# Performance work log

Measured on AMD Instinct MI355X. Metric: run time of the kernel, lower is better.

The kernel has to match this reference:

```python
import jax, jax.numpy as jnp
import numpy as np
from jax import lax

E = 1024      # embed_dim
H = 16        # num_heads
HD = E // H   # head_dim = 64
GS = 2        # head_group_size
G = H // GS   # num head groups = 8
KQ = 3        # kq kernel q size
KK = 3        # kq kernel k size


def setup_inputs() -> dict:
    key = jax.random.key(0)
    ks = jax.random.split(key, 18)
    B, S = 2, 1024
    def rn(k, shape, scale=1.0):
        return jax.random.normal(k, shape, dtype=jnp.float32) * scale
    return {
        "Q": rn(ks[0], (B, S, E)),
        "K": rn(ks[1], (B, S, E)),
        "V": rn(ks[2], (B, S, E)),
        "Wq": rn(ks[3], (E, E), 0.02), "bq": rn(ks[4], (E,), 0.02),
        "Wk": rn(ks[5], (E, E), 0.02), "bk": rn(ks[6], (E,), 0.02),
        "Wv": rn(ks[7], (E, E), 0.02), "bv": rn(ks[8], (E,), 0.02),
        "Wo": rn(ks[9], (E, E), 0.02), "bo": rn(ks[10], (E,), 0.02),
        # depthwise key-query conv: [out=H, in/groups=1, KQ, KK]
        "kq_w": rn(ks[11], (H, 1, KQ, KK), 0.1),
        "kq_b": rn(ks[12], (H,), 0.02),
        # grouped 1x1 head-mix conv: weight [H, GS] (kernel dim squeezed), bias [H]
        "mix_w": rn(ks[13], (H, GS), 0.3),
        "mix_b": rn(ks[14], (H,), 0.02),
        # DynamicTanh params over head_dim (channels_last)
        "dyt_alpha": jnp.array([0.5], dtype=jnp.float32),
        "dyt_w": jnp.ones((HD,), dtype=jnp.float32),
        "dyt_b": jnp.zeros((HD,), dtype=jnp.float32),
        "depth_scale": jnp.ones((1,), dtype=jnp.float32),
    }


def reference(Q, K, V, Wq, bq, Wk, bk, Wv, bv, Wo, bo,
              kq_w, kq_b, mix_w, mix_b, dyt_alpha, dyt_w, dyt_b, depth_scale):
    B, S, _ = Q.shape
    scale = HD ** (-0.5)
    # projections -> [B, H, S, HD]
    q = (Q @ Wq + bq).reshape(B, S, H, HD).transpose(0, 2, 1, 3)
    k = (K @ Wk + bk).reshape(B, S, H, HD).transpose(0, 2, 1, 3)
    v = (V @ Wv + bv).reshape(B, S, H, HD).transpose(0, 2, 1, 3)

    # raw logits [B, H, Sq, Sk], multiplicative causal mask (zeros above diag)
    logits = jnp.einsum('bhqd,bhkd->bhqk', q, k) * scale
    causal = jnp.tril(jnp.ones((S, S), dtype=logits.dtype))
    logits = logits * causal

    # per-head (depthwise) key-query conv2d; torch pads q-dim by 2 both sides
    # then crops to first S rows (causal in q), k-dim padded symmetrically by 1
    conv = lax.conv_general_dilated(
        logits, kq_w, window_strides=(1, 1),
        padding=[(KQ - 1, KQ - 1), ((KK - 1) // 2, (KK - 1) // 2)],
        dimension_numbers=('NCHW', 'OIHW', 'NCHW'),
        feature_group_count=H)
    conv = conv + kq_b[None, :, None, None]
    conv = conv[:, :, :S, :]

    attn = jax.nn.softmax(conv, axis=-1)

    # grouped 1x1 head-mixing conv (within groups of GS heads) + bias
    attn_g = attn.reshape(B, G, GS, S, S)
    mw = mix_w.reshape(G, GS, GS)  # [group, out_in_group, in_in_group]
    mixed = jnp.einsum('goj,bgjqk->bgoqk', mw, attn_g).reshape(B, H, S, S)
    mixed = mixed + mix_b[None, :, None, None]

    out = jnp.einsum('bhqk,bhkd->bhqd', mixed, v)
    # DynamicTanh over head_dim (channels_last) + depth scale
    out = jnp.tanh(dyt_alpha * out) * dyt_w + dyt_b
    out = out * depth_scale
    out = out.transpose(0, 2, 1, 3).reshape(B, S, E)
    return out @ Wo + bo
```

## Files before the change

### kernel.cpp

```cpp
#include <hip/hip_runtime.h>
#include <cstdint>
#include <cstddef>

typedef __bf16 bf16;
typedef __bf16 bf16x8 __attribute__((ext_vector_type(8)));
typedef float f32x4 __attribute__((ext_vector_type(4)));

#define DEVI static __device__ __forceinline__

DEVI unsigned int cvt_pk_bf16(float lo, float hi) {
  unsigned int bl = __float_as_uint(lo);
  bl += 0x7fffu + ((bl >> 16) & 1u);
  unsigned int bh = __float_as_uint(hi);
  bh += 0x7fffu + ((bh >> 16) & 1u);
  return (bl >> 16) | (bh & 0xffff0000u);
}
DEVI float bf_lo(unsigned int u) { return __uint_as_float(u << 16); }
DEVI float bf_hi(unsigned int u) { return __uint_as_float(u & 0xffff0000u); }

DEVI void gload16(const bf16* g, bf16* l) {
  __builtin_amdgcn_global_load_lds(
      (const __attribute__((address_space(1))) unsigned int*)g,
      (__attribute__((address_space(3))) unsigned int*)l, 16, 0, 0);
}

__global__ __launch_bounds__(256) void prep_k(
    const float* __restrict__ Wq, const float* __restrict__ Wk,
    const float* __restrict__ Wv, const float* __restrict__ Wo,
    const float* __restrict__ Q, const float* __restrict__ K,
    const float* __restrict__ V, bf16* __restrict__ Wt,
    bf16* __restrict__ Ab)
{
  __shared__ bf16 Ts[64 * 72];
  const int bid = blockIdx.x, tid = threadIdx.x;
  if (bid < 1024) {
    const int z = bid >> 8;
    const float* W = (z == 0) ? Wq : (z == 1) ? Wk : (z == 2) ? Wv : Wo;
    bf16* out = Wt + ((size_t)z << 20);
    const int n0 = (bid & 15) * 64, k0 = ((bid >> 4) & 15) * 64;
    #pragma unroll
    for (int i = 0; i < 4; ++i) {
      int t = tid + i * 256;
      int kr = t >> 4, nc = t & 15;
      float4 v = *(const float4*)(W + (size_t)(k0 + kr) * 1024 + n0 + nc * 4);
      Ts[(nc * 4 + 0) * 72 + kr] = (bf16)v.x;
      Ts[(nc * 4 + 1) * 72 + kr] = (bf16)v.y;
      Ts[(nc * 4 + 2) * 72 + kr] = (bf16)v.z;
      Ts[(nc * 4 + 3) * 72 + kr] = (bf16)v.w;
    }
    __syncthreads();
    const int n = tid >> 2, kc = tid & 3;
    *(uint4*)(out + (size_t)(n0 + n) * 1024 + k0 + kc * 16) =
        *(const uint4*)(&Ts[n * 72 + kc * 16]);
    *(uint4*)(out + (size_t)(n0 + n) * 1024 + k0 + kc * 16 + 8) =
        *(const uint4*)(&Ts[n * 72 + kc * 16 + 8]);
  } else {
    const int t = bid - 1024;
    const int z = t >> 10, x = t & 1023;
    const float* A = (z == 0) ? Q : (z == 1) ? K : V;
    bf16* o = Ab + ((size_t)z << 21);
    const size_t idx = (size_t)x * 256 + tid;
    const float4 v0 = *(const float4*)(A + idx * 8);
    const float4 v1 = *(const float4*)(A + idx * 8 + 4);
    uint4 u;
    u.x = cvt_pk_bf16(v0.x, v0.y);
    u.y = cvt_pk_bf16(v0.z, v0.w);
    u.z = cvt_pk_bf16(v1.x, v1.y);
    u.w = cvt_pk_bf16(v1.z, v1.w);
    *(uint4*)(o + idx * 8) = u;
  }
}

__global__ __launch_bounds__(256) void proj_gemm_k(
    const bf16* __restrict__ Ab, const bf16* __restrict__ Wt,
    const float* __restrict__ bq, const float* __restrict__ bk,
    const float* __restrict__ bv, bf16* __restrict__ outbase,
    float* __restrict__ Tsum)
{
  const int z = blockIdx.z;
  const bf16* A  = Ab + ((size_t)z << 21);
  const bf16* Bt = Wt + ((size_t)z << 20);
  const float* bias = (z == 0) ? bq : (z == 1) ? bk : bv;
  bf16* outb = outbase + ((size_t)z << 21);

  __shared__ __align__(16) bf16 Asm[2][8192];
  __shared__ __align__(16) bf16 Bsm[2][4096];

  const int tid = threadIdx.x, lane = tid & 63, wid = tid >> 6;
  const int q4 = lane >> 4, n16 = lane & 15;
  const int wm = wid >> 1, wn = wid & 1;
  const int bid = blockIdx.x;
  const int m0 = (bid & 15) * 128, n0 = (bid >> 4) * 64;

  const int cbase = wid * 64 + lane;
  const bf16* gA[4];
  #pragma unroll
  for (int i = 0; i < 4; ++i) {
    int cc = cbase + i * 256;
    gA[i] = A + (size_t)(m0 + (cc >> 3)) * 1024 + (((cc & 7) ^ ((cc >> 3) & 7)) << 3);
  }
  const bf16* gB[2];
  #pragma unroll
  for (int i = 0; i < 2; ++i) {
    int cc = cbase + i * 256;
    gB[i] = Bt + (size_t)(n0 + (cc >> 3)) * 1024 + (((cc & 7) ^ ((cc >> 3) & 7)) << 3);
  }
  const int swl = n16 & 7;

  f32x4 acc[4][2] = {};

  #pragma unroll
  for (int i = 0; i < 4; ++i) gload16(gA[i], &Asm[0][i * 2048 + wid * 512]);
  #pragma unroll
  for (int i = 0; i < 2; ++i) gload16(gB[i], &Bsm[0][i * 2048 + wid * 512]);
  __syncthreads();

  int cur = 0;
  for (int t = 0; t < 16; ++t) {
    if (t < 15) {
      const int kc = (t + 1) * 64;
      #pragma unroll
      for (int i = 0; i < 4; ++i) gload16(gA[i] + kc, &Asm[cur ^ 1][i * 2048 + wid * 512]);
      #pragma unroll
      for (int i = 0; i < 2; ++i) gload16(gB[i] + kc, &Bsm[cur ^ 1][i * 2048 + wid * 512]);
    }
    const char* ab = (const char*)&Asm[cur][0];
    const char* bb = (const char*)&Bsm[cur][0];
    bf16x8 af[2][4], bfv[2][2];
    #pragma unroll
    for (int kk2 = 0; kk2 < 2; ++kk2) {
      #pragma unroll
      for (int rt = 0; rt < 4; ++rt)
        af[kk2][rt] = *(const bf16x8*)(ab + (wm * 64 + rt * 16 + n16) * 128 +
                                       (((kk2 * 4 + q4) ^ swl) << 4));
      #pragma unroll
      for (int ct = 0; ct < 2; ++ct)
        bfv[kk2][ct] = *(const bf16x8*)(bb + (wn * 32 + ct * 16 + n16) * 128 +
                                        (((kk2 * 4 + q4) ^ swl) << 4));
    }
    #pragma unroll
    for (int kk2 = 0; kk2 < 2; ++kk2)
      #pragma unroll
      for (int rt = 0; rt < 4; ++rt)
        #pragma unroll
        for (int ct = 0; ct < 2; ++ct)
          acc[rt][ct] = __builtin_amdgcn_mfma_f32_16x16x32_bf16(af[kk2][rt], bfv[kk2][ct], acc[rt][ct], 0, 0, 0);
    __syncthreads();
    cur ^= 1;
  }

  if (z < 2) {
    const int h = n0 >> 6;
    #pragma unroll
    for (int ct = 0; ct < 2; ++ct) {
      const int dl = wn * 32 + ct * 16 + n16;
      const float bvl = bias[n0 + dl];
      #pragma unroll
      for (int rt = 0; rt < 4; ++rt) {
        #pragma unroll
        for (int r = 0; r < 4; ++r) {
          int row = m0 + wm * 64 + rt * 16 + q4 * 4 + r;
          int b2 = row >> 10, s = row & 1023;
          outb[((size_t)((b2 * 16 + h) * 1024 + s) << 6) + dl] =
              (bf16)(acc[rt][ct][r] + bvl);
        }
      }
    }
  } else {
    const int b2 = m0 >> 10, kt0 = (m0 & 1023) >> 6, hh = n0 >> 6;
    bf16* vout = outb + ((size_t)(b2 * 16 + hh) << 16) + (size_t)(kt0 + wm) * 4096;
    float csum[2] = {0.f, 0.f};
    #pragma unroll
    for (int rt = 0; rt < 4; ++rt) {
      const int kk = rt >> 1;
      const int q4c = (rt & 1) * 2 + (q4 >> 1);
      const int jo = (q4 & 1) * 4;
      #pragma unroll
      for (int ct = 0; ct < 2; ++ct) {
        const int cl = wn * 32 + ct * 16 + n16;
        const float bvl = bias[n0 + cl];
        unsigned int p0 = cvt_pk_bf16(acc[rt][ct][0] + bvl, acc[rt][ct][1] + bvl);
        unsigned int p1 = cvt_pk_bf16(acc[rt][ct][2] + bvl, acc[rt][ct][3] + bvl);
        csum[ct] += bf_lo(p0) + bf_hi(p0) + bf_lo(p1) + bf_hi(p1);
        *(uint2*)(vout + kk * 2048 + (wn * 2 + ct) * 512 + (q4c * 16 + n16) * 8 + jo) =
            make_uint2(p0, p1);
      }
    }
    #pragma unroll
    for (int ct = 0; ct < 2; ++ct) {
      csum[ct] += __shfl_xor(csum[ct], 16);
      csum[ct] += __shfl_xor(csum[ct], 32);
    }
    if (lane < 16) {
      float* tsd = Tsum + ((size_t)(b2 * 16 + hh) * 16 + kt0 + wm) * 64 + wn * 32 + n16;
      tsd[0]  = csum[0];
      tsd[16] = csum[1];
    }
  }
}

__global__ __launch_bounds__(256) void out_gemm_k(
    const bf16* __restrict__ Ab, const bf16* __restrict__ Bt,
    const float* __restrict__ bias, float* __restrict__ outf)
{
  __shared__ __align__(16) bf16 Asm[2][4096];
  __shared__ __align__(16) bf16 Bsm[2][4096];
  const int tid = threadIdx.x, lane = tid & 63, wid = tid >> 6;
  const int q4 = lane >> 4, n16 = lane & 15;
  const int wm = wid >> 1, wn = wid & 1;
  const int bid = blockIdx.x;
  const int m0 = (bid & 31) * 64, n0 = (bid >> 5) * 64;
  const int cbase = wid * 64 + lane;
  const bf16* gA[2];
  const bf16* gB[2];
  #pragma unroll
  for (int i = 0; i < 2; ++i) {
    int cc = cbase + i * 256;
    gA[i] = Ab + (size_t)(m0 + (cc >> 3)) * 1024 + (((cc & 7) ^ ((cc >> 3) & 7)) << 3);
    gB[i] = Bt + (size_t)(n0 + (cc >> 3)) * 1024 + (((cc & 7) ^ ((cc >> 3) & 7)) << 3);
  }
  const int swl = n16 & 7;
  f32x4 acc[2][2] = {};

  #pragma unroll
  for (int i = 0; i < 2; ++i) {
    gload16(gA[i], &Asm[0][i * 2048 + wid * 512]);
    gload16(gB[i], &Bsm[0][i * 2048 + wid * 512]);
  }
  __syncthreads();

  int cur = 0;
  for (int t = 0; t < 16; ++t) {
    if (t < 15) {
      const int kc = (t + 1) * 64;
      #pragma unroll
      for (int i = 0; i < 2; ++i) {
        gload16(gA[i] + kc, &Asm[cur ^ 1][i * 2048 + wid * 512]);
        gload16(gB[i] + kc, &Bsm[cur ^ 1][i * 2048 + wid * 512]);
      }
    }
    const char* ab = (const char*)&Asm[cur][0];
    const char* bb = (const char*)&Bsm[cur][0];
    bf16x8 af[2][2], bfv[2][2];
    #pragma unroll
    for (int kk2 = 0; kk2 < 2; ++kk2) {
      #pragma unroll
      for (int rt = 0; rt < 2; ++rt)
        af[kk2][rt] = *(const bf16x8*)(ab + (wm * 32 + rt * 16 + n16) * 128 +
                                       (((kk2 * 4 + q4) ^ swl) << 4));
      #pragma unroll
      for (int ct = 0; ct < 2; ++ct)
        bfv[kk2][ct] = *(const bf16x8*)(bb + (wn * 32 + ct * 16 + n16) * 128 +
                                        (((kk2 * 4 + q4) ^ swl) << 4));
    }
    #pragma unroll
    for (int kk2 = 0; kk2 < 2; ++kk2)
      #pragma unroll
      for (int rt = 0; rt < 2; ++rt)
        #pragma unroll
        for (int ct = 0; ct < 2; ++ct)
          acc[rt][ct] = __builtin_amdgcn_mfma_f32_16x16x32_bf16(af[kk2][rt], bfv[kk2][ct], acc[rt][ct], 0, 0, 0);
    __syncthreads();
    cur ^= 1;
  }
  #pragma unroll
  for (int ct = 0; ct < 2; ++ct) {
    int col = n0 + wn * 32 + ct * 16 + n16;
    float bvl = bias[col];
    #pragma unroll
    for (int rt = 0; rt < 2; ++rt)
      #pragma unroll
      for (int r = 0; r < 4; ++r) {
        int row = m0 + wm * 32 + rt * 16 + q4 * 4 + r;
        outf[(size_t)row * 1024 + col] = acc[rt][ct][r] + bvl;
      }
  }
}

__global__ __launch_bounds__(320) void logits_conv_k(
    const bf16* __restrict__ qh, const bf16* __restrict__ kh,
    const float* __restrict__ kq_w, const float* __restrict__ kq_b,
    bf16* __restrict__ conv_out, float* __restrict__ tstats,
    const float* __restrict__ Tsum, float* __restrict__ Vtail)
{
  const int tt = blockIdx.x;
  const int h = blockIdx.y, b = blockIdx.z;
  if (tt == 151) {
    const int d = threadIdx.x;
    if (d < 64) {
      float* vt = Vtail + (size_t)(b * 16 + h) * 17 * 64;
      vt[16 * 64 + d] = 0.f;
      float c = 0.f;
      for (int kt = 15; kt >= 0; --kt) {
        c += Tsum[((size_t)(b * 16 + h) * 16 + kt) * 64 + d];
        vt[kt * 64 + d] = c;
      }
    }
    return;
  }
  int qt = 0, base = 0;
  while (qt < 15 && base + qt + 2 <= tt) { base += qt + 2; ++qt; }
  const int ct = tt - base;
  const int q0 = qt * 64, c0 = ct * 64;
  __shared__ __align__(16) char un[19456];
  bf16* Kst = (bf16*)un;
  float* Ls = (float*)un;
  const int tid = threadIdx.x;
  const int lane = tid & 63, wid = tid >> 6;
  const int q4 = lane >> 4, n16 = lane & 15;
  const bf16* qb = qh + ((size_t)(b * 16 + h) << 16);
  const bf16* kb = kh + ((size_t)(b * 16 + h) << 16);

  const int ar = min(max(q0 - 2 + wid * 16 + n16, 0), 1023);
  bf16x8 a0 = *(const bf16x8*)(qb + ar * 64 + q4 * 8);
  bf16x8 a1 = *(const bf16x8*)(qb + ar * 64 + 32 + q4 * 8);

  for (int t = tid; t < 640; t += 320) {
    int row = t >> 3, ch = t & 7;
    int br = min(max(c0 - 1 + row, 0), 1023);
    *(uint4*)(&Kst[row * 72 + ch * 8]) = *(const uint4*)(kb + br * 64 + ch * 8);
  }
  __syncthreads();

  f32x4 acc[5] = {};
  #pragma unroll
  for (int c5 = 0; c5 < 5; ++c5) {
    int brow = c5 * 16 + n16;
    bf16x8 b0 = *(const bf16x8*)(&Kst[brow * 72 + q4 * 8]);
    bf16x8 b1 = *(const bf16x8*)(&Kst[brow * 72 + 32 + q4 * 8]);
    acc[c5] = __builtin_amdgcn_mfma_f32_16x16x32_bf16(a0, b0, acc[c5], 0, 0, 0);
    acc[c5] = __builtin_amdgcn_mfma_f32_16x16x32_bf16(a1, b1, acc[c5], 0, 0, 0);
  }
  __syncthreads();

  #pragma unroll
  for (int c5 = 0; c5 < 5; ++c5) {
    #pragma unroll
    for (int r = 0; r < 4; ++r) {
      int Lrow = wid * 16 + q4 * 4 + r;
      int Lcol = c5 * 16 + n16;
      if (Lrow < 66 && Lcol < 66) {
        int rg = q0 - 2 + Lrow;
        int cg = c0 - 1 + Lcol;
        float v = (cg >= 0 && cg <= rg) ? acc[c5][r] * 0.125f : 0.f;
        Ls[Lrow * 72 + Lcol] = v;
      }
    }
  }
  __syncthreads();

  if (tid < 256) {
    float w9[9];
    #pragma unroll
    for (int i = 0; i < 9; ++i) w9[i] = kq_w[h * 9 + i];
    const float bb = kq_b[h];
    const size_t tplane = (size_t)(b * 16 + h) * 151 + base + ct;
    bf16* tb = conv_out + tplane * 4096;
    float2* st = (float2*)tstats + tplane * 64;

    const int r = tid >> 2, qr = tid & 3;
    float4 R0[5], R1[5], R2[5];
    const float* L0 = &Ls[r * 72 + qr * 16];
    #pragma unroll
    for (int i = 0; i < 5; ++i) {
      R0[i] = *(const float4*)(L0 + i * 4);
      R1[i] = *(const float4*)(L0 + 72 + i * 4);
      R2[i] = *(const float4*)(L0 + 144 + i * 4);
    }
    const float* f0 = (const float*)R0;
    const float* f1 = (const float*)R1;
    const float* f2 = (const float*)R2;
    float o[16];
    #pragma unroll
    for (int jj = 0; jj < 16; ++jj)
      o[jj] = bb + w9[0]*f0[jj] + w9[1]*f0[jj+1] + w9[2]*f0[jj+2]
                 + w9[3]*f1[jj] + w9[4]*f1[jj+1] + w9[5]*f1[jj+2]
                 + w9[6]*f2[jj] + w9[7]*f2[jj+1] + w9[8]*f2[jj+2];
    float mx = o[0];
    #pragma unroll
    for (int jj = 1; jj < 16; ++jj) mx = fmaxf(mx, o[jj]);
    mx = fmaxf(mx, __shfl_xor(mx, 1));
    mx = fmaxf(mx, __shfl_xor(mx, 2));
    unsigned int p[8];
    #pragma unroll
    for (int jj = 0; jj < 8; ++jj)
      p[jj] = cvt_pk_bf16(__expf(o[2*jj] - mx), __expf(o[2*jj+1] - mx));
    const int kk = qr >> 1, q4b = (qr & 1) * 2, sr = r >> 4, n16r = r & 15;
    *(uint4*)(tb + (sr * 2 + kk) * 512 + (q4b * 16 + n16r) * 8)       = *(const uint4*)&p[0];
    *(uint4*)(tb + (sr * 2 + kk) * 512 + ((q4b + 1) * 16 + n16r) * 8) = *(const uint4*)&p[4];
    float s = 0.f;
    #pragma unroll
    for (int jj = 0; jj < 8; ++jj) s += bf_lo(p[jj]) + bf_hi(p[jj]);
    s += __shfl_xor(s, 1);
    s += __shfl_xor(s, 2);
    if (qr == 0) st[r] = make_float2(mx, s);
  }
}

__global__ __launch_bounds__(256) void pv_k(
    const bf16* __restrict__ conv_out, const bf16* __restrict__ V2,
    const float* __restrict__ tstats, const float* __restrict__ Vtail,
    const float* __restrict__ mix_w, const float* __restrict__ mix_b,
    const float* __restrict__ kq_b,
    const float* __restrict__ dyt_alpha, const float* __restrict__ dyt_w,
    const float* __restrict__ dyt_b, const float* __restrict__ depth_scale,
    bf16* __restrict__ out_attn)
{
  const int qt16 = blockIdx.x, g = blockIdx.y, b = blockIdx.z;
  const int qt = qt16 >> 2;
  const int nkt = min(qt + 2, 16);
  const int Tc = 1024 - (nkt << 6);
  const int tid = threadIdx.x, lane = tid & 63, wid = tid >> 6;
  const int q4 = lane >> 4, n16 = lane & 15;
  const int h0 = 2 * g;
  const int sr = qt16 & 3, strow = sr * 16;
  const size_t tbase = (size_t)(qt * (qt + 3) / 2);

  __shared__ float2 rsS[2][16];
  if (tid < 32) {
    const int hh = tid >> 4, rw = tid & 15;
    const float2* tsp = (const float2*)tstats +
        ((size_t)(b * 16 + h0 + hh) * 151 + tbase) * 64 + strow + rw;
    const float kb2 = kq_b[h0 + hh];
    float mx = (Tc > 0) ? kb2 : -3.0e38f;
    for (int kt = 0; kt < nkt; ++kt) mx = fmaxf(mx, tsp[(size_t)kt * 64].x);
    float s = (float)Tc * __expf(kb2 - mx);
    for (int kt = 0; kt < nkt; ++kt) {
      float2 v = tsp[(size_t)kt * 64];
      s += v.y * __expf(v.x - mx);
    }
    rsS[hh][rw] = make_float2(mx, 1.f / s);
  }
  __syncthreads();

  const float m0v = rsS[0][n16].x, m1v = rsS[1][n16].x;
  const float ri0 = rsS[0][n16].y, ri1 = rsS[1][n16].y;
  const float c00 = mix_w[(h0 + 0) * 2 + 0] * ri0, c01 = mix_w[(h0 + 0) * 2 + 1] * ri1;
  const float c10 = mix_w[(h0 + 1) * 2 + 0] * ri0, c11 = mix_w[(h0 + 1) * 2 + 1] * ri1;

  const bf16* pb0 = conv_out +
      ((size_t)(b * 16 + h0) * 151 + tbase) * 4096 + sr * 1024 + lane * 8;
  const bf16* pb1 = pb0 + (size_t)151 * 4096;
  const float2* ts0 = (const float2*)tstats +
      ((size_t)(b * 16 + h0) * 151 + tbase) * 64 + strow + n16;
  const float2* ts1 = ts0 + (size_t)151 * 64;
  const bf16* vb0 = V2 + ((size_t)(b * 16 + h0) << 16) + lane * 8;
  const bf16* vb1 = vb0 + ((size_t)1 << 16);

  f32x4 acc0[4] = {}, acc1[4] = {};
  for (int kt = wid; kt < nkt; kt += 4) {
    uint4 u0[2], u1[2];
    #pragma unroll
    for (int kk = 0; kk < 2; ++kk) {
      u0[kk] = *(const uint4*)(pb0 + (size_t)kt * 4096 + kk * 512);
      u1[kk] = *(const uint4*)(pb1 + (size_t)kt * 4096 + kk * 512);
    }
    const float e0 = __expf(ts0[(size_t)kt * 64].x - m0v);
    const float e1 = __expf(ts1[(size_t)kt * 64].x - m1v);
    const float w00 = c00 * e0, w01 = c01 * e1;
    const float w10 = c10 * e0, w11 = c11 * e1;
    #pragma unroll
    for (int kk = 0; kk < 2; ++kk) {
      bf16x8 bv0[4], bv1[4];
      #pragma unroll
      for (int ctt = 0; ctt < 4; ++ctt) {
        bv0[ctt] = *(const bf16x8*)(vb0 + (size_t)kt * 4096 + kk * 2048 + ctt * 512);
        bv1[ctt] = *(const bf16x8*)(vb1 + (size_t)kt * 4096 + kk * 2048 + ctt * 512);
      }
      bf16x8 af0, af1;
      const unsigned int* a0p = (const unsigned int*)&u0[kk];
      const unsigned int* a1p = (const unsigned int*)&u1[kk];
      #pragma unroll
      for (int i2 = 0; i2 < 4; ++i2) {
        const float plo = bf_lo(a0p[i2]), phi = bf_hi(a0p[i2]);
        const float qlo = bf_lo(a1p[i2]), qhi = bf_hi(a1p[i2]);
        ((unsigned int*)&af0)[i2] = cvt_pk_bf16(w00 * plo + w01 * qlo,
                                                w00 * phi + w01 * qhi);
        ((unsigned int*)&af1)[i2] = cvt_pk_bf16(w10 * plo + w11 * qlo,
                                                w10 * phi + w11 * qhi);
      }
      #pragma unroll
      for (int ctt = 0; ctt < 4; ++ctt) {
        acc0[ctt] = __builtin_amdgcn_mfma_f32_16x16x32_bf16(af0, bv0[ctt], acc0[ctt], 0, 0, 0);
        acc1[ctt] = __builtin_amdgcn_mfma_f32_16x16x32_bf16(af1, bv1[ctt], acc1[ctt], 0, 0, 0);
      }
    }
  }

  __shared__ float Ps[8][16][65];
  #pragma unroll
  for (int ctt = 0; ctt < 4; ++ctt)
    #pragma unroll
    for (int r = 0; r < 4; ++r) {
      Ps[wid * 2 + 0][q4 * 4 + r][ctt * 16 + n16] = acc0[ctt][r];
      Ps[wid * 2 + 1][q4 * 4 + r][ctt * 16 + n16] = acc1[ctt][r];
    }
  __syncthreads();

  const int o = tid >> 7, rem = tid & 127, row = rem >> 3, cg = rem & 7;
  const float2 sA = rsS[0][row], sB = rsS[1][row];
  const float kqb0 = kq_b[h0], kqb1 = kq_b[h0 + 1];
  const float mwa = mix_w[(h0 + o) * 2 + 0], mwb = mix_w[(h0 + o) * 2 + 1];
  const float twr = (Tc > 0) ? (mwa * sA.y * __expf(kqb0 - sA.x) +
                                mwb * sB.y * __expf(kqb1 - sB.x)) : 0.f;
  const float mb = mix_b[h0 + o];
  const float alpha = dyt_alpha[0], dsc = depth_scale[0];
  const float* vt = Vtail + (size_t)(b * 16 + h0 + o) * 17 * 64;
  bf16 outv[8];
  #pragma unroll
  for (int j = 0; j < 8; ++j) {
    const int d = cg * 8 + j;
    float s = Ps[0 * 2 + o][row][d] + Ps[1 * 2 + o][row][d] +
              Ps[2 * 2 + o][row][d] + Ps[3 * 2 + o][row][d];
    float v = s + twr * vt[(size_t)nkt * 64 + d] + mb * vt[d];
    float e = __expf(2.f * alpha * v);
    float th = 1.f - 2.f / (e + 1.f);
    float y = (th * dyt_w[d] + dyt_b[d]) * dsc;
    outv[j] = (bf16)y;
  }
  const int qr = qt16 * 16 + row;
  *(uint4*)(out_attn + (((size_t)(b * 1024 + qr)) << 10) + (h0 + o) * 64 + cg * 8) =
      *(const uint4*)outv;
}

extern "C" void kernel_launch(void* const* d_in, const int* in_sizes, int n_in,
                              void* d_out, int out_size, void* d_ws, size_t ws_size,
                              hipStream_t stream) {
  const float* Q    = (const float*)d_in[0];
  const float* Kx   = (const float*)d_in[1];
  const float* V    = (const float*)d_in[2];
  const float* Wq   = (const float*)d_in[3];
  const float* bq   = (const float*)d_in[4];
  const float* Wk   = (const float*)d_in[5];
  const float* bk   = (const float*)d_in[6];
  const float* Wv   = (const float*)d_in[7];
  const float* bv   = (const float*)d_in[8];
  const float* Wo   = (const float*)d_in[9];
  const float* bo   = (const float*)d_in[10];
  const float* kq_w = (const float*)d_in[11];
  const float* kq_b = (const float*)d_in[12];
  const float* mixw = (const float*)d_in[13];
  const float* mixb = (const float*)d_in[14];
  const float* dyta = (const float*)d_in[15];
  const float* dytw = (const float*)d_in[16];
  const float* dytb = (const float*)d_in[17];
  const float* dsc  = (const float*)d_in[18];

  char* ws = (char*)d_ws;
  bf16* qh     = (bf16*)(ws);
  float* tstat = (float*)(ws + (size_t)(12 << 20));
  float* Vtail = (float*)(ws + (size_t)(16 << 20));
  float* Tsum  = (float*)(ws + (size_t)(16 << 20) + (256 << 10));
  bf16* WtT    = (bf16*)(ws + (size_t)(17 << 20));
  bf16* oat    = (bf16*)(ws + (size_t)(17 << 20));
  bf16* conv   = (bf16*)(ws + (size_t)(25 << 20));
  bf16* Ab     = (bf16*)(ws + (size_t)(25 << 20));
  bf16* kh     = qh + ((size_t)1 << 21);
  bf16* V2     = qh + ((size_t)2 << 21);

  prep_k<<<dim3(4096), 256, 0, stream>>>(Wq, Wk, Wv, Wo, Q, Kx, V, WtT, Ab);
  proj_gemm_k<<<dim3(256, 1, 3), 256, 0, stream>>>(Ab, WtT, bq, bk, bv, qh, Tsum);
  logits_conv_k<<<dim3(152, 16, 2), 320, 0, stream>>>(qh, kh, kq_w, kq_b, conv, tstat,
                                                      Tsum, Vtail);
  pv_k<<<dim3(64, 8, 2), 256, 0, stream>>>(conv, V2, tstat, Vtail, mixw, mixb, kq_b,
                                           dyta, dytw, dytb, dsc, oat);
  out_gemm_k<<<dim3(512), 256, 0, stream>>>(oat, WtT + ((size_t)3 << 20), bo, (float*)d_out);
}
```

Before: 209.6 us.

## Fuse logits, conv, softmax and PV into a flash-style online-softmax kernel

Replaces the two-pass design, which wrote bf16 conv tiles and per-tile stats to global memory and reread them in a separate PV kernel, with one kernel per (query tile, head). That kernel loops over key tiles, keeps the softmax normalised online, and multiplies P by V for both its own head and its pair head. A small mix kernel then applies the grouped head mixing, the DynamicTanh and the tail corrections. This removes the large intermediate traffic. In exchange the grid shrinks to 512 blocks with an uneven causal workload, each key-tile step has serial barriers, P·V work doubles, and fp32 Xs/Xc buffers are written out.

```diff
diff --git a/kernel.cpp b/kernel.cpp
--- a/kernel.cpp
+++ b/kernel.cpp
@@ -277,250 +277,235 @@
   }
 }
 
-__global__ __launch_bounds__(320) void logits_conv_k(
+__global__ __launch_bounds__(320) void fattn_k(
     const bf16* __restrict__ qh, const bf16* __restrict__ kh,
-    const float* __restrict__ kq_w, const float* __restrict__ kq_b,
-    bf16* __restrict__ conv_out, float* __restrict__ tstats,
-    const float* __restrict__ Tsum, float* __restrict__ Vtail)
+    const bf16* __restrict__ V2, const float* __restrict__ kq_w,
+    const float* __restrict__ kq_b, const float* __restrict__ Tsum,
+    float* __restrict__ Xs, float* __restrict__ Xc)
 {
-  const int tt = blockIdx.x;
   const int h = blockIdx.y, b = blockIdx.z;
-  if (tt == 151) {
-    const int d = threadIdx.x;
-    if (d < 64) {
-      float* vt = Vtail + (size_t)(b * 16 + h) * 17 * 64;
-      vt[16 * 64 + d] = 0.f;
-      float c = 0.f;
-      for (int kt = 15; kt >= 0; --kt) {
-        c += Tsum[((size_t)(b * 16 + h) * 16 + kt) * 64 + d];
-        vt[kt * 64 + d] = c;
-      }
-    }
-    return;
-  }
-  int qt = 0, base = 0;
-  while (qt < 15 && base + qt + 2 <= tt) { base += qt + 2; ++qt; }
-  const int ct = tt - base;
-  const int q0 = qt * 64, c0 = ct * 64;
+  const int ph = h ^ 1;
+  const int qt = b ? (15 - blockIdx.x) : blockIdx.x;
+  const int q0 = qt * 64;
+  const int nkt = min(qt + 2, 16);
+  const int Tc = 1024 - (nkt << 6);
   __shared__ __align__(16) char un[19456];
   bf16* Kst = (bf16*)un;
   float* Ls = (float*)un;
-  const int tid = threadIdx.x;
-  const int lane = tid & 63, wid = tid >> 6;
+  __shared__ __align__(16) bf16 Pls[4096];
+  __shared__ float mLds[64], lLds[64], fLds[64], vtnLds[64], vtn2Lds[64];
+
+  const int tid = threadIdx.x, lane = tid & 63, wid = tid >> 6;
   const int q4 = lane >> 4, n16 = lane & 15;
   const bf16* qb = qh + ((size_t)(b * 16 + h) << 16);
-  const bf16* kb = kh + ((size_t)(b * 16 + h) << 16);
+  const bf16* kp = kh + ((size_t)(b * 16 + h) << 16);
+  const bf16* vb  = V2 + ((size_t)(b * 16 + h)  << 16) + lane * 8;
+  const bf16* vb2 = V2 + ((size_t)(b * 16 + ph) << 16) + lane * 8;
+  const float kqb = kq_b[h];
 
   const int ar = min(max(q0 - 2 + wid * 16 + n16, 0), 1023);
   bf16x8 a0 = *(const bf16x8*)(qb + ar * 64 + q4 * 8);
   bf16x8 a1 = *(const bf16x8*)(qb + ar * 64 + 32 + q4 * 8);
 
-  for (int t = tid; t < 640; t += 320) {
-    int row = t >> 3, ch = t & 7;
-    int br = min(max(c0 - 1 + row, 0), 1023);
-    *(uint4*)(&Kst[row * 72 + ch * 8]) = *(const uint4*)(kb + br * 64 + ch * 8);
-  }
+  float w9[9];
+  #pragma unroll
+  for (int i = 0; i < 9; ++i) w9[i] = kq_w[h * 9 + i];
+
+  if (tid < 64) {
+    mLds[tid] = -3.0e38f;
+    lLds[tid] = 0.f;
+    float s = 0.f, s2 = 0.f;
+    for (int k2 = nkt; k2 < 16; ++k2) {
+      s  += Tsum[((size_t)(b * 16 + h)  * 16 + k2) * 64 + tid];
+      s2 += Tsum[((size_t)(b * 16 + ph) * 16 + k2) * 64 + tid];
+    }
+    vtnLds[tid] = s;
+    vtn2Lds[tid] = s2;
+  }
+  f32x4 accp[4] = {}, accq[4] = {};
   __syncthreads();
 
-  f32x4 acc[5] = {};
-  #pragma unroll
-  for (int c5 = 0; c5 < 5; ++c5) {
-    int brow = c5 * 16 + n16;
-    bf16x8 b0 = *(const bf16x8*)(&Kst[brow * 72 + q4 * 8]);
-    bf16x8 b1 = *(const bf16x8*)(&Kst[brow * 72 + 32 + q4 * 8]);
-    acc[c5] = __builtin_amdgcn_mfma_f32_16x16x32_bf16(a0, b0, acc[c5], 0, 0, 0);
-    acc[c5] = __builtin_amdgcn_mfma_f32_16x16x32_bf16(a1, b1, acc[c5], 0, 0, 0);
-  }
-  __syncthreads();
-
-  #pragma unroll
-  for (int c5 = 0; c5 < 5; ++c5) {
-    #pragma unroll
-    for (int r = 0; r < 4; ++r) {
-      int Lrow = wid * 16 + q4 * 4 + r;
-      int Lcol = c5 * 16 + n16;
-      if (Lrow < 66 && Lcol < 66) {
-        int rg = q0 - 2 + Lrow;
-        int cg = c0 - 1 + Lcol;
-        float v = (cg >= 0 && cg <= rg) ? acc[c5][r] * 0.125f : 0.f;
-        Ls[Lrow * 72 + Lcol] = v;
-      }
-    }
-  }
-  __syncthreads();
+  for (int kt = 0; kt < nkt; ++kt) {
+    const int c0 = kt * 64;
+    for (int t = tid; t < 640; t += 320) {
+      int row = t >> 3, ch = t & 7;
+      int br = min(max(c0 - 1 + row, 0), 1023);
+      *(uint4*)(&Kst[row * 72 + ch * 8]) = *(const uint4*)(kp + br * 64 + ch * 8);
+    }
+    __syncthreads();
+
+    f32x4 acc[5] = {};
+    #pragma unroll
+    for (int c5 = 0; c5 < 5; ++c5) {
+      int brow = c5 * 16 + n16;
+      bf16x8 b0 = *(const bf16x8*)(&Kst[brow * 72 + q4 * 8]);
+      bf16x8 b1 = *(const bf16x8*)(&Kst[brow * 72 + 32 + q4 * 8]);
+      acc[c5] = __builtin_amdgcn_mfma_f32_16x16x32_bf16(a0, b0, acc[c5], 0, 0, 0);
+      acc[c5] = __builtin_amdgcn_mfma_f32_16x16x32_bf16(a1, b1, acc[c5], 0, 0, 0);
+    }
+    __syncthreads();
+
+    #pragma unroll
+    for (int c5 = 0; c5 < 5; ++c5) {
+      #pragma unroll
+      for (int r = 0; r < 4; ++r) {
+        int Lrow = wid * 16 + q4 * 4 + r;
+        int Lcol = c5 * 16 + n16;
+        if (Lrow < 66 && Lcol < 66) {
+          int rg = q0 - 2 + Lrow;
+          int cg = c0 - 1 + Lcol;
+          float v = (cg >= 0 && cg <= rg) ? acc[c5][r] * 0.125f : 0.f;
+          Ls[Lrow * 72 + Lcol] = v;
+        }
+      }
+    }
+    __syncthreads();
+
+    if (tid < 256) {
+      const int r = tid >> 2, qr = tid & 3;
+      float4 R0[5], R1[5], R2[5];
+      const float* L0 = &Ls[r * 72 + qr * 16];
+      #pragma unroll
+      for (int i = 0; i < 5; ++i) {
+        R0[i] = *(const float4*)(L0 + i * 4);
+        R1[i] = *(const float4*)(L0 + 72 + i * 4);
+        R2[i] = *(const float4*)(L0 + 144 + i * 4);
+      }
+      const float* f0 = (const float*)R0;
+      const float* f1 = (const float*)R1;
+      const float* f2 = (const float*)R2;
+      float o[16];
+      #pragma unroll
+      for (int jj = 0; jj < 16; ++jj)
+        o[jj] = kqb + w9[0]*f0[jj] + w9[1]*f0[jj+1] + w9[2]*f0[jj+2]
+                    + w9[3]*f1[jj] + w9[4]*f1[jj+1] + w9[5]*f1[jj+2]
+                    + w9[6]*f2[jj] + w9[7]*f2[jj+1] + w9[8]*f2[jj+2];
+      float mx = o[0];
+      #pragma unroll
+      for (int jj = 1; jj < 16; ++jj) mx = fmaxf(mx, o[jj]);
+      mx = fmaxf(mx, __shfl_xor(mx, 1));
+      mx = fmaxf(mx, __shfl_xor(mx, 2));
+      const float m_old = mLds[r];
+      const float m_new = fmaxf(m_old, mx);
+      const float fsc = __expf(m_old - m_new);
+      unsigned int p[8];
+      #pragma unroll
+      for (int jj = 0; jj < 8; ++jj)
+        p[jj] = cvt_pk_bf16(__expf(o[2*jj] - m_new), __expf(o[2*jj+1] - m_new));
+      const int kk = qr >> 1, q4b = (qr & 1) * 2, sr = r >> 4, n16r = r & 15;
+      *(uint4*)(Pls + (sr * 2 + kk) * 512 + (q4b * 16 + n16r) * 8)       = *(const uint4*)&p[0];
+      *(uint4*)(Pls + (sr * 2 + kk) * 512 + ((q4b + 1) * 16 + n16r) * 8) = *(const uint4*)&p[4];
+      float s = 0.f;
+      #pragma unroll
+      for (int jj = 0; jj < 8; ++jj) s += bf_lo(p[jj]) + bf_hi(p[jj]);
+      s += __shfl_xor(s, 1);
+      s += __shfl_xor(s, 2);
+      if (qr == 0) {
+        lLds[r] = lLds[r] * fsc + s;
+        mLds[r] = m_new;
+        fLds[r] = fsc;
+      }
+    }
+    __syncthreads();
+
+    if (tid < 256) {
+      const float fr0 = fLds[wid * 16 + q4 * 4 + 0];
+      const float fr1 = fLds[wid * 16 + q4 * 4 + 1];
+      const float fr2 = fLds[wid * 16 + q4 * 4 + 2];
+      const float fr3 = fLds[wid * 16 + q4 * 4 + 3];
+      #pragma unroll
+      for (int ctt = 0; ctt < 4; ++ctt) {
+        accp[ctt][0] *= fr0; accp[ctt][1] *= fr1;
+        accp[ctt][2] *= fr2; accp[ctt][3] *= fr3;
+        accq[ctt][0] *= fr0; accq[ctt][1] *= fr1;
+        accq[ctt][2] *= fr2; accq[ctt][3] *= fr3;
+      }
+      bf16x8 pa0 = *(const bf16x8*)(Pls + (wid * 2 + 0) * 512 + lane * 8);
+      bf16x8 pa1 = *(const bf16x8*)(Pls + (wid * 2 + 1) * 512 + lane * 8);
+      #pragma unroll
+      for (int ctt = 0; ctt < 4; ++ctt) {
+        bf16x8 bv0 = *(const bf16x8*)(vb + (size_t)kt * 4096 + ctt * 512);
+        bf16x8 bv1 = *(const bf16x8*)(vb + (size_t)kt * 4096 + 2048 + ctt * 512);
+        accp[ctt] = __builtin_amdgcn_mfma_f32_16x16x32_bf16(pa0, bv0, accp[ctt], 0, 0, 0);
+        accp[ctt] = __builtin_amdgcn_mfma_f32_16x16x32_bf16(pa1, bv1, accp[ctt], 0, 0, 0);
+        bf16x8 cv0 = *(const bf16x8*)(vb2 + (size_t)kt * 4096 + ctt * 512);
+        bf16x8 cv1 = *(const bf16x8*)(vb2 + (size_t)kt * 4096 + 2048 + ctt * 512);
+        accq[ctt] = __builtin_amdgcn_mfma_f32_16x16x32_bf16(pa0, cv0, accq[ctt], 0, 0, 0);
+        accq[ctt] = __builtin_amdgcn_mfma_f32_16x16x32_bf16(pa1, cv1, accq[ctt], 0, 0, 0);
+      }
+    }
+  }
 
   if (tid < 256) {
-    float w9[9];
-    #pragma unroll
-    for (int i = 0; i < 9; ++i) w9[i] = kq_w[h * 9 + i];
-    const float bb = kq_b[h];
-    const size_t tplane = (size_t)(b * 16 + h) * 151 + base + ct;
-    bf16* tb = conv_out + tplane * 4096;
-    float2* st = (float2*)tstats + tplane * 64;
-
-    const int r = tid >> 2, qr = tid & 3;
-    float4 R0[5], R1[5], R2[5];
-    const float* L0 = &Ls[r * 72 + qr * 16];
-    #pragma unroll
-    for (int i = 0; i < 5; ++i) {
-      R0[i] = *(const float4*)(L0 + i * 4);
-      R1[i] = *(const float4*)(L0 + 72 + i * 4);
-      R2[i] = *(const float4*)(L0 + 144 + i * 4);
-    }
-    const float* f0 = (const float*)R0;
-    const float* f1 = (const float*)R1;
-    const float* f2 = (const float*)R2;
-    float o[16];
-    #pragma unroll
-    for (int jj = 0; jj < 16; ++jj)
-      o[jj] = bb + w9[0]*f0[jj] + w9[1]*f0[jj+1] + w9[2]*f0[jj+2]
-                 + w9[3]*f1[jj] + w9[4]*f1[jj+1] + w9[5]*f1[jj+2]
-                 + w9[6]*f2[jj] + w9[7]*f2[jj+1] + w9[8]*f2[jj+2];
-    float mx = o[0];
-    #pragma unroll
-    for (int jj = 1; jj < 16; ++jj) mx = fmaxf(mx, o[jj]);
-    mx = fmaxf(mx, __shfl_xor(mx, 1));
-    mx = fmaxf(mx, __shfl_xor(mx, 2));
-    unsigned int p[8];
-    #pragma unroll
-    for (int jj = 0; jj < 8; ++jj)
-      p[jj] = cvt_pk_bf16(__expf(o[2*jj] - mx), __expf(o[2*jj+1] - mx));
-    const int kk = qr >> 1, q4b = (qr & 1) * 2, sr = r >> 4, n16r = r & 15;
-    *(uint4*)(tb + (sr * 2 + kk) * 512 + (q4b * 16 + n16r) * 8)       = *(const uint4*)&p[0];
-    *(uint4*)(tb + (sr * 2 + kk) * 512 + ((q4b + 1) * 16 + n16r) * 8) = *(const uint4*)&p[4];
-    float s = 0.f;
-    #pragma unroll
-    for (int jj = 0; jj < 8; ++jj) s += bf_lo(p[jj]) + bf_hi(p[jj]);
-    s += __shfl_xor(s, 1);
-    s += __shfl_xor(s, 2);
-    if (qr == 0) st[r] = make_float2(mx, s);
-  }
-}
-
-__global__ __launch_bounds__(256) void pv_k(
-    const bf16* __restrict__ conv_out, const bf16* __restrict__ V2,
-    const float* __restrict__ tstats, const float* __restrict__ Vtail,
+    float* As = Xs + ((size_t)(b * 16 + h) << 16);
+    float* Ac = Xc + ((size_t)(b * 16 + h) << 16);
+    #pragma unroll
+    for (int rr = 0; rr < 4; ++rr) {
+      const int row = wid * 16 + q4 * 4 + rr;
+      const float m_run = mLds[row], l_run = lLds[row];
+      float g = 1.f, eb = 0.f, l = l_run;
+      if (Tc > 0) {
+        const float mf = fmaxf(m_run, kqb);
+        g = __expf(m_run - mf);
+        eb = __expf(kqb - mf);
+        l = l_run * g + (float)Tc * eb;
+      }
+      const float rinv = 1.f / l;
+      #pragma unroll
+      for (int ctt = 0; ctt < 4; ++ctt) {
+        const int col = ctt * 16 + n16;
+        As[(size_t)(q0 + row) * 64 + col] =
+            (accp[ctt][rr] * g + eb * vtnLds[col]) * rinv;
+        Ac[(size_t)(q0 + row) * 64 + col] =
+            (accq[ctt][rr] * g + eb * vtn2Lds[col]) * rinv;
+      }
+    }
+  }
+}
+
+__global__ __launch_bounds__(256) void mix_k(
+    const float* __restrict__ Xs, const float* __restrict__ Xc,
+    const float* __restrict__ Tsum,
     const float* __restrict__ mix_w, const float* __restrict__ mix_b,
-    const float* __restrict__ kq_b,
     const float* __restrict__ dyt_alpha, const float* __restrict__ dyt_w,
     const float* __restrict__ dyt_b, const float* __restrict__ depth_scale,
-    bf16* __restrict__ out_attn)
+    bf16* __restrict__ oat)
 {
-  const int qt16 = blockIdx.x, g = blockIdx.y, b = blockIdx.z;
-  const int qt = qt16 >> 2;
-  const int nkt = min(qt + 2, 16);
-  const int Tc = 1024 - (nkt << 6);
-  const int tid = threadIdx.x, lane = tid & 63, wid = tid >> 6;
-  const int q4 = lane >> 4, n16 = lane & 15;
-  const int h0 = 2 * g;
-  const int sr = qt16 & 3, strow = sr * 16;
-  const size_t tbase = (size_t)(qt * (qt + 3) / 2);
-
-  __shared__ float2 rsS[2][16];
-  if (tid < 32) {
-    const int hh = tid >> 4, rw = tid & 15;
-    const float2* tsp = (const float2*)tstats +
-        ((size_t)(b * 16 + h0 + hh) * 151 + tbase) * 64 + strow + rw;
-    const float kb2 = kq_b[h0 + hh];
-    float mx = (Tc > 0) ? kb2 : -3.0e38f;
-    for (int kt = 0; kt < nkt; ++kt) mx = fmaxf(mx, tsp[(size_t)kt * 64].x);
-    float s = (float)Tc * __expf(kb2 - mx);
-    for (int kt = 0; kt < nkt; ++kt) {
-      float2 v = tsp[(size_t)kt * 64];
-      s += v.y * __expf(v.x - mx);
-    }
-    rsS[hh][rw] = make_float2(mx, 1.f / s);
+  const int qc = blockIdx.x, h = blockIdx.y, b = blockIdx.z;
+  const int tid = threadIdx.x;
+  __shared__ float vt0[64];
+  if (tid < 64) {
+    float s = 0.f;
+    for (int kt = 0; kt < 16; ++kt)
+      s += Tsum[((size_t)(b * 16 + h) * 16 + kt) * 64 + tid];
+    vt0[tid] = s;
   }
   __syncthreads();
-
-  const float m0v = rsS[0][n16].x, m1v = rsS[1][n16].x;
-  const float ri0 = rsS[0][n16].y, ri1 = rsS[1][n16].y;
-  const float c00 = mix_w[(h0 + 0) * 2 + 0] * ri0, c01 = mix_w[(h0 + 0) * 2 + 1] * ri1;
-  const float c10 = mix_w[(h0 + 1) * 2 + 0] * ri0, c11 = mix_w[(h0 + 1) * 2 + 1] * ri1;
-
-  const bf16* pb0 = conv_out +
-      ((size_t)(b * 16 + h0) * 151 + tbase) * 4096 + sr * 1024 + lane * 8;
-  const bf16* pb1 = pb0 + (size_t)151 * 4096;
-  const float2* ts0 = (const float2*)tstats +
-      ((size_t)(b * 16 + h0) * 151 + tbase) * 64 + strow + n16;
-  const float2* ts1 = ts0 + (size_t)151 * 64;
-  const bf16* vb0 = V2 + ((size_t)(b * 16 + h0) << 16) + lane * 8;
-  const bf16* vb1 = vb0 + ((size_t)1 << 16);
-
-  f32x4 acc0[4] = {}, acc1[4] = {};
-  for (int kt = wid; kt < nkt; kt += 4) {
-    uint4 u0[2], u1[2];
-    #pragma unroll
-    for (int kk = 0; kk < 2; ++kk) {
-      u0[kk] = *(const uint4*)(pb0 + (size_t)kt * 4096 + kk * 512);
-      u1[kk] = *(const uint4*)(pb1 + (size_t)kt * 4096 + kk * 512);
-    }
-    const float e0 = __expf(ts0[(size_t)kt * 64].x - m0v);
-    const float e1 = __expf(ts1[(size_t)kt * 64].x - m1v);
-    const float w00 = c00 * e0, w01 = c01 * e1;
-    const float w10 = c10 * e0, w11 = c11 * e1;
-    #pragma unroll
-    for (int kk = 0; kk < 2; ++kk) {
-      bf16x8 bv0[4], bv1[4];
-      #pragma unroll
-      for (int ctt = 0; ctt < 4; ++ctt) {
-        bv0[ctt] = *(const bf16x8*)(vb0 + (size_t)kt * 4096 + kk * 2048 + ctt * 512);
-        bv1[ctt] = *(const bf16x8*)(vb1 + (size_t)kt * 4096 + kk * 2048 + ctt * 512);
-      }
-      bf16x8 af0, af1;
-      const unsigned int* a0p = (const unsigned int*)&u0[kk];
-      const unsigned int* a1p = (const unsigned int*)&u1[kk];
-      #pragma unroll
-      for (int i2 = 0; i2 < 4; ++i2) {
-        const float plo = bf_lo(a0p[i2]), phi = bf_hi(a0p[i2]);
-        const float qlo = bf_lo(a1p[i2]), qhi = bf_hi(a1p[i2]);
-        ((unsigned int*)&af0)[i2] = cvt_pk_bf16(w00 * plo + w01 * qlo,
-                                                w00 * phi + w01 * qhi);
-        ((unsigned int*)&af1)[i2] = cvt_pk_bf16(w10 * plo + w11 * qlo,
-                                                w10 * phi + w11 * qhi);
-      }
-      #pragma unroll
-      for (int ctt = 0; ctt < 4; ++ctt) {
-        acc0[ctt] = __builtin_amdgcn_mfma_f32_16x16x32_bf16(af0, bv0[ctt], acc0[ctt], 0, 0, 0);
-        acc1[ctt] = __builtin_amdgcn_mfma_f32_16x16x32_bf16(af1, bv1[ctt], acc1[ctt], 0, 0, 0);
-      }
-    }
-  }
-
-  __shared__ float Ps[8][16][65];
-  #pragma unroll
-  for (int ctt = 0; ctt < 4; ++ctt)
-    #pragma unroll
-    for (int r = 0; r < 4; ++r) {
-      Ps[wid * 2 + 0][q4 * 4 + r][ctt * 16 + n16] = acc0[ctt][r];
-      Ps[wid * 2 + 1][q4 * 4 + r][ctt * 16 + n16] = acc1[ctt][r];
-    }
-  __syncthreads();
-
-  const int o = tid >> 7, rem = tid & 127, row = rem >> 3, cg = rem & 7;
-  const float2 sA = rsS[0][row], sB = rsS[1][row];
-  const float kqb0 = kq_b[h0], kqb1 = kq_b[h0 + 1];
-  const float mwa = mix_w[(h0 + o) * 2 + 0], mwb = mix_w[(h0 + o) * 2 + 1];
-  const float twr = (Tc > 0) ? (mwa * sA.y * __expf(kqb0 - sA.x) +
-                                mwb * sB.y * __expf(kqb1 - sB.x)) : 0.f;
-  const float mb = mix_b[h0 + o];
+  const int j0 = h & ~1, j1 = j0 + 1;
+  const float* A0 = ((h & 1) ? Xc : Xs) + ((size_t)(b * 16 + j0) << 16);
+  const float* A1 = ((h & 1) ? Xs : Xc) + ((size_t)(b * 16 + j1) << 16);
+  const float mw0 = mix_w[h * 2 + 0], mw1 = mix_w[h * 2 + 1], mbv = mix_b[h];
   const float alpha = dyt_alpha[0], dsc = depth_scale[0];
-  const float* vt = Vtail + (size_t)(b * 16 + h0 + o) * 17 * 64;
-  bf16 outv[8];
-  #pragma unroll
-  for (int j = 0; j < 8; ++j) {
-    const int d = cg * 8 + j;
-    float s = Ps[0 * 2 + o][row][d] + Ps[1 * 2 + o][row][d] +
-              Ps[2 * 2 + o][row][d] + Ps[3 * 2 + o][row][d];
-    float v = s + twr * vt[(size_t)nkt * 64 + d] + mb * vt[d];
-    float e = __expf(2.f * alpha * v);
-    float th = 1.f - 2.f / (e + 1.f);
-    float y = (th * dyt_w[d] + dyt_b[d]) * dsc;
-    outv[j] = (bf16)y;
-  }
-  const int qr = qt16 * 16 + row;
-  *(uint4*)(out_attn + (((size_t)(b * 1024 + qr)) << 10) + (h0 + o) * 64 + cg * 8) =
-      *(const uint4*)outv;
+  const int d0 = (tid & 15) * 4;
+  const int qoff = tid >> 4;
+  for (int rep = 0; rep < 8; ++rep) {
+    const int q = qc * 128 + rep * 16 + qoff;
+    const float4 u0 = *(const float4*)(A0 + (size_t)q * 64 + d0);
+    const float4 u1 = *(const float4*)(A1 + (size_t)q * 64 + d0);
+    const float* a0p = (const float*)&u0;
+    const float* a1p = (const float*)&u1;
+    bf16 outv[4];
+    #pragma unroll
+    for (int i = 0; i < 4; ++i) {
+      const int d = d0 + i;
+      float v = mw0 * a0p[i] + mw1 * a1p[i] + mbv * vt0[d];
+      float e = __expf(2.f * alpha * v);
+      float th = 1.f - 2.f / (e + 1.f);
+      outv[i] = (bf16)((th * dyt_w[d] + dyt_b[d]) * dsc);
+    }
+    *(uint2*)(oat + ((size_t)(b * 1024 + q) << 10) + h * 64 + d0) =
+        *(const uint2*)outv;
+  }
 }
 
 extern "C" void kernel_launch(void* const* d_in, const int* in_sizes, int n_in,
@@ -548,21 +533,19 @@
 
   char* ws = (char*)d_ws;
   bf16* qh     = (bf16*)(ws);
-  float* tstat = (float*)(ws + (size_t)(12 << 20));
-  float* Vtail = (float*)(ws + (size_t)(16 << 20));
   float* Tsum  = (float*)(ws + (size_t)(16 << 20) + (256 << 10));
   bf16* WtT    = (bf16*)(ws + (size_t)(17 << 20));
   bf16* oat    = (bf16*)(ws + (size_t)(17 << 20));
-  bf16* conv   = (bf16*)(ws + (size_t)(25 << 20));
   bf16* Ab     = (bf16*)(ws + (size_t)(25 << 20));
+  float* Xs    = (float*)(ws + (size_t)(25 << 20));
+  float* Xc    = (float*)(ws + (size_t)(33 << 20));
   bf16* kh     = qh + ((size_t)1 << 21);
   bf16* V2     = qh + ((size_t)2 << 21);
 
   prep_k<<<dim3(4096), 256, 0, stream>>>(Wq, Wk, Wv, Wo, Q, Kx, V, WtT, Ab);
   proj_gemm_k<<<dim3(256, 1, 3), 256, 0, stream>>>(Ab, WtT, bq, bk, bv, qh, Tsum);
-  logits_conv_k<<<dim3(152, 16, 2), 320, 0, stream>>>(qh, kh, kq_w, kq_b, conv, tstat,
-                                                      Tsum, Vtail);
-  pv_k<<<dim3(64, 8, 2), 256, 0, stream>>>(conv, V2, tstat, Vtail, mixw, mixb, kq_b,
-                                           dyta, dytw, dytb, dsc, oat);
+  fattn_k<<<dim3(16, 16, 2), 320, 0, stream>>>(qh, kh, V2, kq_w, kq_b, Tsum, Xs, Xc);
+  mix_k<<<dim3(8, 16, 2), 256, 0, stream>>>(Xs, Xc, Tsum, mixw, mixb,
+                                            dyta, dytw, dytb, dsc, oat);
   out_gemm_k<<<dim3(512), 256, 0, stream>>>(oat, WtT + ((size_t)3 << 20), bo, (float*)d_out);
 }
```

After: 225.2 us. +7.5%, slower.
